# Kernel optimization log

Hardware: AMD Instinct MI355X
Metric: run time of the kernel (lower is better)

The kernel has to match this reference:

```python
import jax, jax.numpy as jnp
import numpy as np

B, L, D_IN = 2, 4096, 512
H, D_K, D_V, D_OUT = 8, 64, 64, 512


def setup_inputs() -> dict:
    key = jax.random.key(0)
    k0, k1, k2, k3, k4 = jax.random.split(key, 5)
    x = jax.random.normal(k0, (B, L, D_IN), dtype=jnp.float32)
    W_q = jax.random.uniform(k1, (H, D_IN, D_K), dtype=jnp.float32)
    W_k = jax.random.uniform(k2, (H, D_IN, D_K), dtype=jnp.float32)
    W_v = jax.random.uniform(k3, (H, D_IN, D_V), dtype=jnp.float32)
    W_o = jax.random.uniform(k4, (H, D_V, D_OUT), dtype=jnp.float32)
    return {"x": x, "W_q": W_q, "W_k": W_k, "W_v": W_v, "W_o": W_o}


def reference(x, W_q, W_k, W_v, W_o):
    # x: (b, l, d_in); projections per head -> (b, h, l, d)
    Q = jnp.einsum('hjk,blj->bhlk', W_q, x)
    K = jnp.einsum('hjk,blj->bhlk', W_k, x)
    V = jnp.einsum('hjv,blj->bhlv', W_v, x)
    # no softmax: pure bilinear attention (Q K^T) V
    scores = jnp.einsum('bhik,bhjk->bhij', Q, K)          # (b, h, l, l)
    values = jnp.einsum('bhqk,bhkv->bhqv', scores, V)     # (b, h, l, d_v)
    return jnp.einsum('hvo,bhlv->blo', W_o, values)       # (b, l, d_out)
```

## Files before the change

### kernel.cpp

```cpp
#include <hip/hip_runtime.h>
#include <cstdint>


#define BDIM 2
#define LDIM 4096
#define DIN 512
#define HDIM 8
#define DK 64
#define DV 64
#define DOUT 512

using bf16_t = __bf16;
typedef __bf16 bf16x8 __attribute__((ext_vector_type(8)));
typedef float floatx4 __attribute__((ext_vector_type(4)));

__device__ __forceinline__ unsigned short f2bf(float f) {
    unsigned int u = __builtin_bit_cast(unsigned int, f);
    u += 0x7FFFu + ((u >> 16) & 1u);
    return (unsigned short)(u >> 16);
}

__device__ __forceinline__ void gld_lds16(const void* g, void* l) {
    __builtin_amdgcn_global_load_lds(
        (const __attribute__((address_space(1))) void*)g,
        (__attribute__((address_space(3))) void*)l, 16, 0, 0);
}

template <int BM, int BN, int BK, bool TRANS_OUT, int OUT_MODE>
__device__ __forceinline__ void gemm_core(const bf16_t* A, const bf16_t* B,
                                          void* Cp, int K, int lda, int ldb,
                                          int ldc, int tm, int tn) {
    constexpr int WM = BM / 2, WN = BN / 2;
    constexpr int FM = WM / 16, FN = WN / 16;
    constexpr int CPR = BK / 8;
    __shared__ bf16_t As[BM * BK];
    __shared__ bf16_t Bs[BN * BK];
    const int tid = threadIdx.x;
    const int lane = tid & 63;
    const int wr = (tid >> 7) & 1;
    const int wc = (tid >> 6) & 1;

    A += (size_t)tm * lda;
    B += (size_t)tn * ldb;

    floatx4 acc[FM][FN] = {};

    for (int k0 = 0; k0 < K; k0 += BK) {
#pragma unroll
        for (int i = 0; i < (BM * CPR) / 256; ++i) {
            int c = i * 256 + tid;
            int m = c / CPR, kc = c % CPR;
            gld_lds16(A + (size_t)m * lda + k0 + kc * 8, As + c * 8);
        }
#pragma unroll
        for (int i = 0; i < (BN * CPR) / 256; ++i) {
            int c = i * 256 + tid;
            int m = c / CPR, kc = c % CPR;
            gld_lds16(B + (size_t)m * ldb + k0 + kc * 8, Bs + c * 8);
        }
        __syncthreads();

#pragma unroll
        for (int kk = 0; kk < BK; kk += 32) {
            bf16x8 aF[FM], bF[FN];
#pragma unroll
            for (int fm = 0; fm < FM; ++fm)
                aF[fm] = *(const bf16x8*)(As + (wr * WM + fm * 16 + (lane & 15)) * BK +
                                          kk + (lane >> 4) * 8);
#pragma unroll
            for (int fn = 0; fn < FN; ++fn)
                bF[fn] = *(const bf16x8*)(Bs + (wc * WN + fn * 16 + (lane & 15)) * BK +
                                          kk + (lane >> 4) * 8);
#pragma unroll
            for (int fm = 0; fm < FM; ++fm)
#pragma unroll
                for (int fn = 0; fn < FN; ++fn)
                    acc[fm][fn] = __builtin_amdgcn_mfma_f32_16x16x32_bf16(
                        aF[fm], bF[fn], acc[fm][fn], 0, 0, 0);
        }
        __syncthreads();
    }

    const int cr4 = (lane >> 4) * 4;
    const int cn = lane & 15;
#pragma unroll
    for (int fm = 0; fm < FM; ++fm)
#pragma unroll
        for (int fn = 0; fn < FN; ++fn)
#pragma unroll
            for (int r = 0; r < 4; ++r) {
                int m = tm + wr * WM + fm * 16 + cr4 + r;
                int n = tn + wc * WN + fn * 16 + cn;
                size_t idx = TRANS_OUT ? ((size_t)n * ldc + m)
                                       : ((size_t)m * ldc + n);
                if (OUT_MODE == 0)
                    ((float*)Cp)[idx] = acc[fm][fn][r];
                else
                    ((unsigned short*)Cp)[idx] = f2bf(acc[fm][fn][r]);
            }
}

__global__ __launch_bounds__(256) void k_kvm(const bf16_t* xb16,
                                             const bf16_t* WkvT, float* M32) {
    constexpr int EP = 136;
    __shared__ bf16_t smem[128 * EP];
    bf16_t* As = smem;
    bf16_t* Bs = smem + 128 * 64;
    const int lt = blockIdx.x, h = blockIdx.y, b = blockIdx.z;
    const int tid = threadIdx.x;
    const int lane = tid & 63;
    const int wr = (tid >> 7) & 1, wc = (tid >> 6) & 1;
    const int cr4 = (lane >> 4) * 4, cn = lane & 15;

    const bf16_t* A = xb16 + (size_t)b * LDIM * DIN + (size_t)lt * 128 * DIN;
    const bf16_t* B = WkvT + (size_t)h * 128 * DIN;

    floatx4 acc[4][4] = {};
    for (int k0 = 0; k0 < DIN; k0 += 64) {
#pragma unroll
        for (int i = 0; i < 4; ++i) {
            int c = i * 256 + tid, m = c >> 3, kc = c & 7;
            gld_lds16(A + (size_t)m * DIN + k0 + kc * 8, As + c * 8);
        }
#pragma unroll
        for (int i = 0; i < 4; ++i) {
            int c = i * 256 + tid, m = c >> 3, kc = c & 7;
            gld_lds16(B + (size_t)m * DIN + k0 + kc * 8, Bs + c * 8);
        }
        __syncthreads();
#pragma unroll
        for (int kk = 0; kk < 64; kk += 32) {
            bf16x8 aF[4], bF[4];
#pragma unroll
            for (int fm = 0; fm < 4; ++fm)
                aF[fm] = *(const bf16x8*)(As + (wr * 64 + fm * 16 + cn) * 64 +
                                          kk + (lane >> 4) * 8);
#pragma unroll
            for (int fn = 0; fn < 4; ++fn)
                bF[fn] = *(const bf16x8*)(Bs + (wc * 64 + fn * 16 + cn) * 64 +
                                          kk + (lane >> 4) * 8);
#pragma unroll
            for (int fm = 0; fm < 4; ++fm)
#pragma unroll
                for (int fn = 0; fn < 4; ++fn)
                    acc[fm][fn] = __builtin_amdgcn_mfma_f32_16x16x32_bf16(
                        aF[fm], bF[fn], acc[fm][fn], 0, 0, 0);
        }
        __syncthreads();
    }

#pragma unroll
    for (int fm = 0; fm < 4; ++fm)
#pragma unroll
        for (int fn = 0; fn < 4; ++fn)
#pragma unroll
            for (int r = 0; r < 4; ++r) {
                int m = wr * 64 + fm * 16 + cr4 + r;
                int n = wc * 64 + fn * 16 + cn;
                ((unsigned short*)smem)[n * EP + m] = f2bf(acc[fm][fn][r]);
            }
    __syncthreads();

    floatx4 mm[2][2] = {};
#pragma unroll
    for (int kk = 0; kk < 128; kk += 32) {
        bf16x8 aF[2], bF[2];
#pragma unroll
        for (int f = 0; f < 2; ++f) {
            aF[f] = *(const bf16x8*)(smem + (wr * 32 + f * 16 + cn) * EP + kk +
                                     (lane >> 4) * 8);
            bF[f] = *(const bf16x8*)(smem + (64 + wc * 32 + f * 16 + cn) * EP +
                                     kk + (lane >> 4) * 8);
        }
#pragma unroll
        for (int fm = 0; fm < 2; ++fm)
#pragma unroll
            for (int fn = 0; fn < 2; ++fn)
                mm[fm][fn] = __builtin_amdgcn_mfma_f32_16x16x32_bf16(
                    aF[fm], bF[fn], mm[fm][fn], 0, 0, 0);
    }
    float* Mh = M32 + ((size_t)(b * HDIM + h)) * (DK * DV);
#pragma unroll
    for (int fm = 0; fm < 2; ++fm)
#pragma unroll
        for (int fn = 0; fn < 2; ++fn)
#pragma unroll
            for (int r = 0; r < 4; ++r) {
                int dk = wr * 32 + fm * 16 + cr4 + r;
                int v = wc * 32 + fn * 16 + cn;
                atomicAdd(&Mh[dk * 64 + v], mm[fm][fn][r]);
            }
}

__global__ __launch_bounds__(256) void k_tail(const bf16_t* WqC, const bf16_t* WoT,
                                              const float* M32, unsigned short* CT) {
    int i0 = blockIdx.x * 64, o0 = blockIdx.y * 64, b = blockIdx.z;
    __shared__ bf16_t Aq[64 * 64];
    __shared__ bf16_t Ws[64 * 64];
    __shared__ bf16_t Msh[64 * 64];
    __shared__ bf16_t PTs[64 * 64];
    const int tid = threadIdx.x;
    const int lane = tid & 63;
    const int wr = (tid >> 7) & 1, wc = (tid >> 6) & 1;
    const int cr4 = (lane >> 4) * 4, cn = lane & 15;

    floatx4 acc[2][2] = {};

    for (int h = 0; h < HDIM; ++h) {
#pragma unroll
        for (int i = 0; i < 2; ++i) {
            int c = i * 256 + tid, m = c >> 3, kc = c & 7;
            gld_lds16(WqC + (size_t)(i0 + m) * DIN + h * 64 + kc * 8, Aq + c * 8);
            gld_lds16(WoT + ((size_t)h * DOUT + o0 + m) * DV + kc * 8, Ws + c * 8);
        }
        const float* Mh = M32 + ((size_t)(b * HDIM + h)) * (DK * DV);
#pragma unroll
        for (int i = 0; i < 4; ++i) {
            int idx = (i * 256 + tid) * 4;
            float4 v = *(const float4*)(Mh + idx);
            *(ushort4*)((unsigned short*)Msh + idx) =
                make_ushort4(f2bf(v.x), f2bf(v.y), f2bf(v.z), f2bf(v.w));
        }
        __syncthreads();

        floatx4 pt[2][2] = {};
#pragma unroll
        for (int kk = 0; kk < 64; kk += 32) {
            bf16x8 aF[2], bF[2];
#pragma unroll
            for (int f = 0; f < 2; ++f) {
                aF[f] = *(const bf16x8*)(Ws + (wr * 32 + f * 16 + cn) * 64 + kk +
                                         (lane >> 4) * 8);
                bF[f] = *(const bf16x8*)(Msh + (wc * 32 + f * 16 + cn) * 64 + kk +
                                         (lane >> 4) * 8);
            }
#pragma unroll
            for (int fm = 0; fm < 2; ++fm)
#pragma unroll
                for (int fn = 0; fn < 2; ++fn)
                    pt[fm][fn] = __builtin_amdgcn_mfma_f32_16x16x32_bf16(
                        aF[fm], bF[fn], pt[fm][fn], 0, 0, 0);
        }
#pragma unroll
        for (int fm = 0; fm < 2; ++fm)
#pragma unroll
            for (int fn = 0; fn < 2; ++fn)
#pragma unroll
                for (int r = 0; r < 4; ++r) {
                    int m = wr * 32 + fm * 16 + cr4 + r;
                    int n = wc * 32 + fn * 16 + cn;
                    ((unsigned short*)PTs)[m * 64 + n] = f2bf(pt[fm][fn][r]);
                }
        __syncthreads();

#pragma unroll
        for (int kk = 0; kk < 64; kk += 32) {
            bf16x8 aF[2], bF[2];
#pragma unroll
            for (int f = 0; f < 2; ++f) {
                aF[f] = *(const bf16x8*)(PTs + (wr * 32 + f * 16 + cn) * 64 + kk +
                                         (lane >> 4) * 8);
                bF[f] = *(const bf16x8*)(Aq + (wc * 32 + f * 16 + cn) * 64 + kk +
                                         (lane >> 4) * 8);
            }
#pragma unroll
            for (int fm = 0; fm < 2; ++fm)
#pragma unroll
                for (int fn = 0; fn < 2; ++fn)
                    acc[fm][fn] = __builtin_amdgcn_mfma_f32_16x16x32_bf16(
                        aF[fm], bF[fn], acc[fm][fn], 0, 0, 0);
        }
        __syncthreads();
    }

    unsigned short* CTb = CT + (size_t)b * DIN * DOUT;
#pragma unroll
    for (int fm = 0; fm < 2; ++fm)
#pragma unroll
        for (int fn = 0; fn < 2; ++fn)
#pragma unroll
            for (int r = 0; r < 4; ++r) {
                int m = wr * 32 + fm * 16 + cr4 + r;
                int n = wc * 32 + fn * 16 + cn;
                CTb[(size_t)(o0 + m) * DIN + i0 + n] = f2bf(acc[fm][fn][r]);
            }
}

__global__ __launch_bounds__(256) void k_out(const bf16_t* x16, const bf16_t* CT,
                                             float* out) {
    int b = blockIdx.z;
    gemm_core<64, 128, 64, false, 0>(x16 + (size_t)b * LDIM * DIN,
                                     CT + (size_t)b * DIN * DOUT,
                                     out + (size_t)b * LDIM * DOUT, DIN, DIN,
                                     DIN, DOUT, blockIdx.x * 64,
                                     blockIdx.y * 128);
}

__global__ __launch_bounds__(256) void k_prep2(
    const float* x, const float* Wq, const float* Wk, const float* Wv,
    const float* Wo, unsigned short* xb, unsigned short* WqC,
    unsigned short* WkvT, unsigned short* WoT, float* M32) {
    __shared__ unsigned short T[64][65];
    int tr = threadIdx.x >> 4, tc4 = (threadIdx.x & 15) * 4;
    int bid = blockIdx.x;
    if (bid < 2048) {
        size_t base = ((size_t)bid * 256 + threadIdx.x) * 8;
        float4 v0 = *(const float4*)(x + base);
        float4 v1 = *(const float4*)(x + base + 4);
        unsigned short o[8] = {f2bf(v0.x), f2bf(v0.y), f2bf(v0.z), f2bf(v0.w),
                               f2bf(v1.x), f2bf(v1.y), f2bf(v1.z), f2bf(v1.w)};
        *(uint4*)(xb + base) = *(const uint4*)o;
        return;
    }
    if (bid >= 2304) {
        size_t g = ((size_t)(bid - 2304) * 256 + threadIdx.x) * 32;
        float4 z4 = make_float4(0.f, 0.f, 0.f, 0.f);
#pragma unroll
        for (int q = 0; q < 8; ++q) *(float4*)(M32 + g + q * 4) = z4;
        return;
    }
    int p_ = bid - 2048;
    int t = p_ & 7, job = (p_ >> 3) & 3, h = p_ >> 5;
    if (job == 0) {
        const float* src = Wq + (size_t)h * DIN * DK;
#pragma unroll
        for (int p = 0; p < 4; ++p) {
            int i = t * 64 + p * 16 + tr;
            float4 v = *(const float4*)(src + (size_t)i * DK + tc4);
            *(ushort4*)(WqC + (size_t)i * (HDIM * DK) + h * DK + tc4) =
                make_ushort4(f2bf(v.x), f2bf(v.y), f2bf(v.z), f2bf(v.w));
        }
        return;
    }
    const float* src;
    unsigned short* dst;
    int rows, cols, r0, c0;
    if (job == 1) {
        src = Wk + (size_t)h * DIN * DK;
        dst = WkvT + ((size_t)h * 128) * DIN;
        rows = DIN; cols = DK; r0 = t * 64; c0 = 0;
    } else if (job == 2) {
        src = Wv + (size_t)h * DIN * DV;
        dst = WkvT + ((size_t)h * 128 + 64) * DIN;
        rows = DIN; cols = DV; r0 = t * 64; c0 = 0;
    } else {
        src = Wo + (size_t)h * DV * DOUT;
        dst = WoT + (size_t)h * DOUT * DV;
        rows = DV; cols = DOUT; r0 = 0; c0 = t * 64;
    }
#pragma unroll
    for (int p = 0; p < 4; ++p) {
        int r = p * 16 + tr;
        float4 v = *(const float4*)(src + (size_t)(r0 + r) * cols + c0 + tc4);
        T[r][tc4 + 0] = f2bf(v.x); T[r][tc4 + 1] = f2bf(v.y);
        T[r][tc4 + 2] = f2bf(v.z); T[r][tc4 + 3] = f2bf(v.w);
    }
    __syncthreads();
#pragma unroll
    for (int p = 0; p < 4; ++p) {
        int c = p * 16 + tr;
        ushort4 u = make_ushort4(T[tc4 + 0][c], T[tc4 + 1][c], T[tc4 + 2][c],
                                 T[tc4 + 3][c]);
        *(ushort4*)(dst + (size_t)(c0 + c) * rows + r0 + tc4) = u;
    }
}

extern "C" void kernel_launch(void* const* d_in, const int* in_sizes, int n_in,
                              void* d_out, int out_size, void* d_ws, size_t ws_size,
                              hipStream_t stream) {
    const float* x  = (const float*)d_in[0];
    const float* Wq = (const float*)d_in[1];
    const float* Wk = (const float*)d_in[2];
    const float* Wv = (const float*)d_in[3];
    const float* Wo = (const float*)d_in[4];
    float* out = (float*)d_out;

    unsigned short* w = (unsigned short*)d_ws;
    unsigned short* xb16  = w; w += (size_t)BDIM * LDIM * DIN;
    unsigned short* WqC   = w; w += (size_t)DIN * HDIM * DK;
    unsigned short* WkvT  = w; w += (size_t)1024 * DIN;
    unsigned short* WoT   = w; w += (size_t)HDIM * DOUT * DV;
    unsigned short* CT    = w; w += (size_t)BDIM * DIN * DOUT;
    float* M32 = (float*)(((uintptr_t)w + 255) & ~(uintptr_t)255);

    k_prep2<<<dim3(2312), 256, 0, stream>>>(x, Wq, Wk, Wv, Wo, xb16, WqC,
                                            WkvT, WoT, M32);
    k_kvm<<<dim3(LDIM / 128, HDIM, BDIM), 256, 0, stream>>>(
        (const bf16_t*)xb16, (const bf16_t*)WkvT, M32);
    k_tail<<<dim3(8, 8, BDIM), 256, 0, stream>>>((const bf16_t*)WqC,
                                                 (const bf16_t*)WoT, M32, CT);
    k_out<<<dim3(LDIM / 64, DOUT / 128, BDIM), 256, 0, stream>>>(
        (const bf16_t*)xb16, (const bf16_t*)CT, out);
}
```

Before: 124.6 us.

## Restructure pipeline around Gram matrix X^T X and fused Q projection

Swaps the per-head K^T V accumulation for a per-batch Gram matrix G = X^T X, computed with atomics over L chunks. The last blocks to finish then wait on a global counter and compute M = Wk^T G Wv per head inside the same kernel, while other blocks of that kernel compute the Q projection. The output kernel now applies M and Wo per head to the stored Q rather than going through a precomputed combined weight. The change adds a transposed copy of x, an inter-block spin-wait that assumes all blocks are co-resident, and a new order of bf16 rounding.

```diff
diff --git a/kernel.cpp b/kernel.cpp
--- a/kernel.cpp
+++ b/kernel.cpp
@@ -9,10 +9,23 @@
 #define DK 64
 #define DV 64
 #define DOUT 512
+#define NXTX 512
+#define NMID 32
+#define SMEM_MAIN 34816
 
 using bf16_t = __bf16;
 typedef __bf16 bf16x8 __attribute__((ext_vector_type(8)));
 typedef float floatx4 __attribute__((ext_vector_type(4)));
+
+constexpr size_t OFF_XB  = 4096;
+constexpr size_t OFF_XT  = OFF_XB  + (size_t)BDIM * LDIM * DIN * 2;
+constexpr size_t OFF_WQT = OFF_XT  + (size_t)BDIM * LDIM * DIN * 2;
+constexpr size_t OFF_WKT = OFF_WQT + (size_t)HDIM * DK * DIN * 2;
+constexpr size_t OFF_WVT = OFF_WKT + (size_t)HDIM * DK * DIN * 2;
+constexpr size_t OFF_WOT = OFF_WVT + (size_t)HDIM * DV * DIN * 2;
+constexpr size_t OFF_QP  = OFF_WOT + (size_t)HDIM * DOUT * DV * 2;
+constexpr size_t OFF_G32 = OFF_QP  + (size_t)BDIM * LDIM * DIN * 2;
+constexpr size_t OFF_M32 = OFF_G32 + (size_t)BDIM * DIN * DIN * 4;
 
 __device__ __forceinline__ unsigned short f2bf(float f) {
     unsigned int u = __builtin_bit_cast(unsigned int, f);
@@ -26,15 +39,16 @@
         (__attribute__((address_space(3))) void*)l, 16, 0, 0);
 }
 
-template <int BM, int BN, int BK, bool TRANS_OUT, int OUT_MODE>
-__device__ __forceinline__ void gemm_core(const bf16_t* A, const bf16_t* B,
-                                          void* Cp, int K, int lda, int ldb,
-                                          int ldc, int tm, int tn) {
+template <int BM, int BN, int BK, int OUT_MODE>
+__device__ __forceinline__ void gemm_tn(char* smem, const bf16_t* A,
+                                        const bf16_t* B, void* Cp, int K,
+                                        int lda, int ldb, int ldc, int tm,
+                                        int tn) {
     constexpr int WM = BM / 2, WN = BN / 2;
     constexpr int FM = WM / 16, FN = WN / 16;
     constexpr int CPR = BK / 8;
-    __shared__ bf16_t As[BM * BK];
-    __shared__ bf16_t Bs[BN * BK];
+    bf16_t* As = (bf16_t*)smem;
+    bf16_t* Bs = As + BM * BK;
     const int tid = threadIdx.x;
     const int lane = tid & 63;
     const int wr = (tid >> 7) & 1;
@@ -91,54 +105,343 @@
             for (int r = 0; r < 4; ++r) {
                 int m = tm + wr * WM + fm * 16 + cr4 + r;
                 int n = tn + wc * WN + fn * 16 + cn;
-                size_t idx = TRANS_OUT ? ((size_t)n * ldc + m)
-                                       : ((size_t)m * ldc + n);
-                if (OUT_MODE == 0)
-                    ((float*)Cp)[idx] = acc[fm][fn][r];
+                size_t idx = (size_t)m * ldc + n;
+                if (OUT_MODE == 1)
+                    ((unsigned short*)Cp)[idx] = f2bf(acc[fm][fn][r]);
                 else
-                    ((unsigned short*)Cp)[idx] = f2bf(acc[fm][fn][r]);
-            }
-}
-
-__global__ __launch_bounds__(256) void k_kvm(const bf16_t* xb16,
-                                             const bf16_t* WkvT, float* M32) {
-    constexpr int EP = 136;
-    __shared__ bf16_t smem[128 * EP];
-    bf16_t* As = smem;
-    bf16_t* Bs = smem + 128 * 64;
-    const int lt = blockIdx.x, h = blockIdx.y, b = blockIdx.z;
+                    atomicAdd((float*)Cp + idx, acc[fm][fn][r]);
+            }
+}
+
+__global__ __launch_bounds__(256) void k_prep(
+    const float* __restrict__ x, const float* __restrict__ Wq,
+    const float* __restrict__ Wk, const float* __restrict__ Wv,
+    const float* __restrict__ Wo, char* __restrict__ ws) {
+    __shared__ unsigned short T[64][65];
+    unsigned short* xb  = (unsigned short*)(ws + OFF_XB);
+    unsigned short* xT  = (unsigned short*)(ws + OFF_XT);
+    unsigned short* WqT = (unsigned short*)(ws + OFF_WQT);
+    unsigned short* WkT = (unsigned short*)(ws + OFF_WKT);
+    unsigned short* WvT = (unsigned short*)(ws + OFF_WVT);
+    unsigned short* WoT = (unsigned short*)(ws + OFF_WOT);
+    float* G32 = (float*)(ws + OFF_G32);
+    float* M32 = (float*)(ws + OFF_M32);
+
     const int tid = threadIdx.x;
-    const int lane = tid & 63;
+    const int tr = tid >> 4, tc4 = (tid & 15) * 4;
+    const int j = blockIdx.x;
+
+    if (j < 1024) {
+        const int b = j >> 9, q = j & 511, lt = q >> 3, it = q & 7;
+        const float* src = x + (size_t)b * LDIM * DIN + (size_t)lt * 64 * DIN +
+                           it * 64;
+        unsigned short* d0 = xb + (size_t)b * LDIM * DIN +
+                             (size_t)lt * 64 * DIN + it * 64;
+        unsigned short* d1 = xT + (size_t)b * DIN * LDIM +
+                             (size_t)it * 64 * LDIM + lt * 64;
+#pragma unroll
+        for (int p = 0; p < 4; ++p) {
+            int r = p * 16 + tr;
+            float4 v = *(const float4*)(src + (size_t)r * DIN + tc4);
+            ushort4 u = make_ushort4(f2bf(v.x), f2bf(v.y), f2bf(v.z), f2bf(v.w));
+            *(ushort4*)(d0 + (size_t)r * DIN + tc4) = u;
+            T[r][tc4 + 0] = u.x; T[r][tc4 + 1] = u.y;
+            T[r][tc4 + 2] = u.z; T[r][tc4 + 3] = u.w;
+        }
+        __syncthreads();
+#pragma unroll
+        for (int p = 0; p < 4; ++p) {
+            int c = p * 16 + tr;
+            ushort4 u = make_ushort4(T[tc4 + 0][c], T[tc4 + 1][c], T[tc4 + 2][c],
+                                     T[tc4 + 3][c]);
+            *(ushort4*)(d1 + (size_t)c * LDIM + tc4) = u;
+        }
+        return;
+    }
+    if (j < 1280) {
+        const int q = j - 1024;
+        const int t = q & 7, h = (q >> 3) & 7, typ = q >> 6;
+        const float* src;
+        unsigned short* dst;
+        int rows, cols, r0, c0;
+        if (typ == 0) { src = Wq + (size_t)h * DIN * DK; dst = WqT + (size_t)h * DK * DIN;
+                        rows = DIN; cols = DK; r0 = t * 64; c0 = 0; }
+        else if (typ == 1) { src = Wk + (size_t)h * DIN * DK; dst = WkT + (size_t)h * DK * DIN;
+                        rows = DIN; cols = DK; r0 = t * 64; c0 = 0; }
+        else if (typ == 2) { src = Wv + (size_t)h * DIN * DV; dst = WvT + (size_t)h * DV * DIN;
+                        rows = DIN; cols = DV; r0 = t * 64; c0 = 0; }
+        else { src = Wo + (size_t)h * DV * DOUT; dst = WoT + (size_t)h * DOUT * DV;
+                        rows = DV; cols = DOUT; r0 = 0; c0 = t * 64; }
+#pragma unroll
+        for (int p = 0; p < 4; ++p) {
+            int r = p * 16 + tr;
+            float4 v = *(const float4*)(src + (size_t)(r0 + r) * cols + c0 + tc4);
+            T[r][tc4 + 0] = f2bf(v.x); T[r][tc4 + 1] = f2bf(v.y);
+            T[r][tc4 + 2] = f2bf(v.z); T[r][tc4 + 3] = f2bf(v.w);
+        }
+        __syncthreads();
+#pragma unroll
+        for (int p = 0; p < 4; ++p) {
+            int c = p * 16 + tr;
+            ushort4 u = make_ushort4(T[tc4 + 0][c], T[tc4 + 1][c], T[tc4 + 2][c],
+                                     T[tc4 + 3][c]);
+            *(ushort4*)(dst + (size_t)(c0 + c) * rows + r0 + tc4) = u;
+        }
+        return;
+    }
+    if (j < 1408) {
+        float* g = G32 + (size_t)(j - 1280) * 8192 + tid * 32;
+        float4 z = make_float4(0.f, 0.f, 0.f, 0.f);
+#pragma unroll
+        for (int q = 0; q < 8; ++q) *(float4*)(g + q * 4) = z;
+        return;
+    }
+    {
+        float* m = M32 + (size_t)(j - 1408) * 8192 + tid * 32;
+        float4 z = make_float4(0.f, 0.f, 0.f, 0.f);
+#pragma unroll
+        for (int q = 0; q < 8; ++q) *(float4*)(m + q * 4) = z;
+        if (j == 1408 && tid == 0) *(unsigned*)ws = 0u;
+    }
+}
+
+__device__ void mid_job(int id, char* smem, const bf16_t* WkT,
+                        const bf16_t* WvT, const float* G32, float* M32) {
+    const int tid = threadIdx.x, lane = tid & 63;
     const int wr = (tid >> 7) & 1, wc = (tid >> 6) & 1;
     const int cr4 = (lane >> 4) * 4, cn = lane & 15;
-
-    const bf16_t* A = xb16 + (size_t)b * LDIM * DIN + (size_t)lt * 128 * DIN;
-    const bf16_t* B = WkvT + (size_t)h * 128 * DIN;
+    const int h = id & 7, b = (id >> 3) & 1, jh = (id >> 4) & 1;
+    bf16_t* As  = (bf16_t*)smem;
+    bf16_t* Bs  = (bf16_t*)(smem + 8192);
+    bf16_t* T2s = (bf16_t*)(smem + 16384);
+    bf16_t* Vs  = (bf16_t*)(smem + 25600);
+    const bf16_t* Ah = WkT + (size_t)h * DK * DIN;
+    const bf16_t* Vh = WvT + (size_t)h * DV * DIN;
+    const float* Gb = G32 + (size_t)b * DIN * DIN;
+
+    floatx4 accM[2][2] = {};
+    for (int jt = 0; jt < 4; ++jt) {
+        const int j0 = jh * 256 + jt * 64;
+        floatx4 accT[2][2] = {};
+        for (int k0 = 0; k0 < DIN; k0 += 64) {
+#pragma unroll
+            for (int i = 0; i < 2; ++i) {
+                int c = i * 256 + tid, m = c >> 3, kc = c & 7;
+                gld_lds16(Ah + (size_t)m * DIN + k0 + kc * 8, As + c * 8);
+            }
+#pragma unroll
+            for (int i = 0; i < 2; ++i) {
+                int c = i * 256 + tid, n = c >> 3, kc = c & 7;
+                const float* g = Gb + (size_t)(j0 + n) * DIN + k0 + kc * 8;
+                float4 v0 = *(const float4*)g;
+                float4 v1 = *(const float4*)(g + 4);
+                unsigned short o[8] = {f2bf(v0.x), f2bf(v0.y), f2bf(v0.z),
+                                       f2bf(v0.w), f2bf(v1.x), f2bf(v1.y),
+                                       f2bf(v1.z), f2bf(v1.w)};
+                *(uint4*)((unsigned short*)Bs + (size_t)c * 8) = *(const uint4*)o;
+            }
+            __syncthreads();
+#pragma unroll
+            for (int kk = 0; kk < 64; kk += 32) {
+                bf16x8 aF[2], bF[2];
+#pragma unroll
+                for (int f = 0; f < 2; ++f) {
+                    aF[f] = *(const bf16x8*)(As + (wr * 32 + f * 16 + cn) * 64 +
+                                             kk + (lane >> 4) * 8);
+                    bF[f] = *(const bf16x8*)(Bs + (wc * 32 + f * 16 + cn) * 64 +
+                                             kk + (lane >> 4) * 8);
+                }
+#pragma unroll
+                for (int fm = 0; fm < 2; ++fm)
+#pragma unroll
+                    for (int fn = 0; fn < 2; ++fn)
+                        accT[fm][fn] = __builtin_amdgcn_mfma_f32_16x16x32_bf16(
+                            aF[fm], bF[fn], accT[fm][fn], 0, 0, 0);
+            }
+            __syncthreads();
+        }
+#pragma unroll
+        for (int fm = 0; fm < 2; ++fm)
+#pragma unroll
+            for (int fn = 0; fn < 2; ++fn)
+#pragma unroll
+                for (int r = 0; r < 4; ++r)
+                    ((unsigned short*)T2s)[(wr * 32 + fm * 16 + cr4 + r) * 72 +
+                                           wc * 32 + fn * 16 + cn] =
+                        f2bf(accT[fm][fn][r]);
+#pragma unroll
+        for (int i = 0; i < 2; ++i) {
+            int c = i * 256 + tid, v = c >> 3, kc = c & 7;
+            gld_lds16(Vh + (size_t)v * DIN + j0 + kc * 8, Vs + c * 8);
+        }
+        __syncthreads();
+#pragma unroll
+        for (int kk = 0; kk < 64; kk += 32) {
+            bf16x8 aF[2], bF[2];
+#pragma unroll
+            for (int f = 0; f < 2; ++f) {
+                aF[f] = *(const bf16x8*)(T2s + (wr * 32 + f * 16 + cn) * 72 + kk +
+                                         (lane >> 4) * 8);
+                bF[f] = *(const bf16x8*)(Vs + (wc * 32 + f * 16 + cn) * 64 + kk +
+                                         (lane >> 4) * 8);
+            }
+#pragma unroll
+            for (int fm = 0; fm < 2; ++fm)
+#pragma unroll
+                for (int fn = 0; fn < 2; ++fn)
+                    accM[fm][fn] = __builtin_amdgcn_mfma_f32_16x16x32_bf16(
+                        aF[fm], bF[fn], accM[fm][fn], 0, 0, 0);
+        }
+        __syncthreads();
+    }
+    float* Mh = M32 + (size_t)(b * HDIM + h) * (DK * DV);
+#pragma unroll
+    for (int fm = 0; fm < 2; ++fm)
+#pragma unroll
+        for (int fn = 0; fn < 2; ++fn)
+#pragma unroll
+            for (int r = 0; r < 4; ++r)
+                atomicAdd(&Mh[(wr * 32 + fm * 16 + cr4 + r) * 64 + wc * 32 +
+                              fn * 16 + cn],
+                          accM[fm][fn][r]);
+}
+
+__global__ __launch_bounds__(256) void k_main(char* __restrict__ ws) {
+    __shared__ __align__(16) char smem[SMEM_MAIN];
+    __shared__ int s_old;
+    const bf16_t* xb  = (const bf16_t*)(ws + OFF_XB);
+    const bf16_t* xT  = (const bf16_t*)(ws + OFF_XT);
+    const bf16_t* WqT = (const bf16_t*)(ws + OFF_WQT);
+    const bf16_t* WkT = (const bf16_t*)(ws + OFF_WKT);
+    const bf16_t* WvT = (const bf16_t*)(ws + OFF_WVT);
+    unsigned short* Qp = (unsigned short*)(ws + OFF_QP);
+    float* G32 = (float*)(ws + OFF_G32);
+    float* M32 = (float*)(ws + OFF_M32);
+    unsigned* done = (unsigned*)ws;
+
+    const int bid = blockIdx.x;
+    const int tid = threadIdx.x;
+
+    if (bid < NXTX) {
+        const int b = bid >> 8, r = bid & 255;
+        const int chunk = r >> 6, t = r & 63;
+        const int it = t >> 3, jt = t & 7;
+        const bf16_t* Xb = xT + (size_t)b * DIN * LDIM + chunk * 1024;
+        gemm_tn<64, 64, 64, 2>(smem, Xb, Xb, G32 + (size_t)b * DIN * DIN, 1024,
+                               LDIM, LDIM, DIN, it * 64, jt * 64);
+        __syncthreads();
+        if (tid == 0) {
+            unsigned old = __hip_atomic_fetch_add(done, 1u, __ATOMIC_RELAXED,
+                                                  __HIP_MEMORY_SCOPE_SYSTEM);
+            s_old = (int)old;
+        }
+        __syncthreads();
+        int old = s_old;
+        if (old >= NXTX - NMID) {
+            if (tid == 0) {
+                while (__hip_atomic_load(done, __ATOMIC_RELAXED,
+                                         __HIP_MEMORY_SCOPE_SYSTEM) <
+                       (unsigned)NXTX)
+                    __builtin_amdgcn_s_sleep(8);
+            }
+            __syncthreads();
+            mid_job(old - (NXTX - NMID), smem, WkT, WvT, G32, M32);
+        }
+    } else {
+        const int q = bid - NXTX;
+        const int b = q >> 7, t = q & 127;
+        const int lt = t >> 2, nt = t & 3;
+        gemm_tn<128, 128, 64, 1>(smem, xb + (size_t)b * LDIM * DIN, WqT,
+                                 Qp + (size_t)b * LDIM * (HDIM * DK), DIN, DIN,
+                                 DIN, HDIM * DK, lt * 128, nt * 128);
+    }
+}
+
+__global__ __launch_bounds__(256) void k_out(const char* __restrict__ ws,
+                                             float* __restrict__ out) {
+    __shared__ __align__(16) bf16_t Qs[128 * 64];
+    __shared__ __align__(16) bf16_t Ws[128 * 64];
+    __shared__ __align__(16) bf16_t Ms[64 * 72];
+    __shared__ __align__(16) bf16_t PTs[128 * 72];
+    const bf16_t* WoT = (const bf16_t*)(ws + OFF_WOT);
+    const bf16_t* Qp  = (const bf16_t*)(ws + OFF_QP);
+    const float* M32  = (const float*)(ws + OFF_M32);
+
+    const int lt = blockIdx.x, nt = blockIdx.y, b = blockIdx.z;
+    const int l0 = lt * 128, o0 = nt * 128;
+    const int tid = threadIdx.x, lane = tid & 63;
+    const int wr = (tid >> 7) & 1, wc = (tid >> 6) & 1;
+    const int cr4 = (lane >> 4) * 4, cn = lane & 15;
 
     floatx4 acc[4][4] = {};
-    for (int k0 = 0; k0 < DIN; k0 += 64) {
+
+    for (int h = 0; h < HDIM; ++h) {
+        {
+            const float* Mh = M32 + (size_t)(b * HDIM + h) * (DK * DV);
+            int dk = tid >> 2, v0 = (tid & 3) * 16;
+            const float* s = Mh + dk * 64 + v0;
+            unsigned short o[16];
+#pragma unroll
+            for (int q = 0; q < 4; ++q) {
+                float4 v = *(const float4*)(s + q * 4);
+                o[q * 4 + 0] = f2bf(v.x); o[q * 4 + 1] = f2bf(v.y);
+                o[q * 4 + 2] = f2bf(v.z); o[q * 4 + 3] = f2bf(v.w);
+            }
+            unsigned short* d = (unsigned short*)Ms + dk * 72 + v0;
+            *(uint4*)d = *(const uint4*)o;
+            *(uint4*)(d + 8) = *(const uint4*)(o + 8);
+        }
 #pragma unroll
         for (int i = 0; i < 4; ++i) {
             int c = i * 256 + tid, m = c >> 3, kc = c & 7;
-            gld_lds16(A + (size_t)m * DIN + k0 + kc * 8, As + c * 8);
-        }
-#pragma unroll
-        for (int i = 0; i < 4; ++i) {
-            int c = i * 256 + tid, m = c >> 3, kc = c & 7;
-            gld_lds16(B + (size_t)m * DIN + k0 + kc * 8, Bs + c * 8);
-        }
-        __syncthreads();
+            gld_lds16(WoT + ((size_t)h * DOUT + o0 + m) * DV + kc * 8,
+                      Ws + c * 8);
+            gld_lds16(Qp + (size_t)b * LDIM * 512 + (size_t)(l0 + m) * 512 +
+                          h * 64 + kc * 8,
+                      Qs + c * 8);
+        }
+        __syncthreads();
+
+        floatx4 accP[2][4] = {};
+#pragma unroll
+        for (int kk = 0; kk < 64; kk += 32) {
+            bf16x8 aF[2], bF[4];
+#pragma unroll
+            for (int f = 0; f < 2; ++f)
+                aF[f] = *(const bf16x8*)(Ms + (wr * 32 + f * 16 + cn) * 72 + kk +
+                                         (lane >> 4) * 8);
+#pragma unroll
+            for (int f = 0; f < 4; ++f)
+                bF[f] = *(const bf16x8*)(Ws + (wc * 64 + f * 16 + cn) * 64 + kk +
+                                         (lane >> 4) * 8);
+#pragma unroll
+            for (int fm = 0; fm < 2; ++fm)
+#pragma unroll
+                for (int fn = 0; fn < 4; ++fn)
+                    accP[fm][fn] = __builtin_amdgcn_mfma_f32_16x16x32_bf16(
+                        aF[fm], bF[fn], accP[fm][fn], 0, 0, 0);
+        }
+#pragma unroll
+        for (int fm = 0; fm < 2; ++fm)
+#pragma unroll
+            for (int fn = 0; fn < 4; ++fn)
+#pragma unroll
+                for (int r = 0; r < 4; ++r)
+                    ((unsigned short*)PTs)[(wc * 64 + fn * 16 + cn) * 72 +
+                                           wr * 32 + fm * 16 + cr4 + r] =
+                        f2bf(accP[fm][fn][r]);
+        __syncthreads();
+
 #pragma unroll
         for (int kk = 0; kk < 64; kk += 32) {
             bf16x8 aF[4], bF[4];
 #pragma unroll
-            for (int fm = 0; fm < 4; ++fm)
-                aF[fm] = *(const bf16x8*)(As + (wr * 64 + fm * 16 + cn) * 64 +
-                                          kk + (lane >> 4) * 8);
-#pragma unroll
-            for (int fn = 0; fn < 4; ++fn)
-                bF[fn] = *(const bf16x8*)(Bs + (wc * 64 + fn * 16 + cn) * 64 +
-                                          kk + (lane >> 4) * 8);
+            for (int f = 0; f < 4; ++f) {
+                aF[f] = *(const bf16x8*)(Qs + (wr * 64 + f * 16 + cn) * 64 + kk +
+                                         (lane >> 4) * 8);
+                bF[f] = *(const bf16x8*)(PTs + (wc * 64 + f * 16 + cn) * 72 + kk +
+                                         (lane >> 4) * 8);
+            }
 #pragma unroll
             for (int fm = 0; fm < 4; ++fm)
 #pragma unroll
@@ -149,220 +452,17 @@
         __syncthreads();
     }
 
+    float* ob = out + (size_t)b * LDIM * DOUT;
 #pragma unroll
     for (int fm = 0; fm < 4; ++fm)
 #pragma unroll
         for (int fn = 0; fn < 4; ++fn)
 #pragma unroll
             for (int r = 0; r < 4; ++r) {
-                int m = wr * 64 + fm * 16 + cr4 + r;
-                int n = wc * 64 + fn * 16 + cn;
-                ((unsigned short*)smem)[n * EP + m] = f2bf(acc[fm][fn][r]);
-            }
-    __syncthreads();
-
-    floatx4 mm[2][2] = {};
-#pragma unroll
-    for (int kk = 0; kk < 128; kk += 32) {
-        bf16x8 aF[2], bF[2];
-#pragma unroll
-        for (int f = 0; f < 2; ++f) {
-            aF[f] = *(const bf16x8*)(smem + (wr * 32 + f * 16 + cn) * EP + kk +
-                                     (lane >> 4) * 8);
-            bF[f] = *(const bf16x8*)(smem + (64 + wc * 32 + f * 16 + cn) * EP +
-                                     kk + (lane >> 4) * 8);
-        }
-#pragma unroll
-        for (int fm = 0; fm < 2; ++fm)
-#pragma unroll
-            for (int fn = 0; fn < 2; ++fn)
-                mm[fm][fn] = __builtin_amdgcn_mfma_f32_16x16x32_bf16(
-                    aF[fm], bF[fn], mm[fm][fn], 0, 0, 0);
-    }
-    float* Mh = M32 + ((size_t)(b * HDIM + h)) * (DK * DV);
-#pragma unroll
-    for (int fm = 0; fm < 2; ++fm)
-#pragma unroll
-        for (int fn = 0; fn < 2; ++fn)
-#pragma unroll
-            for (int r = 0; r < 4; ++r) {
-                int dk = wr * 32 + fm * 16 + cr4 + r;
-                int v = wc * 32 + fn * 16 + cn;
-                atomicAdd(&Mh[dk * 64 + v], mm[fm][fn][r]);
-            }
-}
-
-__global__ __launch_bounds__(256) void k_tail(const bf16_t* WqC, const bf16_t* WoT,
-                                              const float* M32, unsigned short* CT) {
-    int i0 = blockIdx.x * 64, o0 = blockIdx.y * 64, b = blockIdx.z;
-    __shared__ bf16_t Aq[64 * 64];
-    __shared__ bf16_t Ws[64 * 64];
-    __shared__ bf16_t Msh[64 * 64];
-    __shared__ bf16_t PTs[64 * 64];
-    const int tid = threadIdx.x;
-    const int lane = tid & 63;
-    const int wr = (tid >> 7) & 1, wc = (tid >> 6) & 1;
-    const int cr4 = (lane >> 4) * 4, cn = lane & 15;
-
-    floatx4 acc[2][2] = {};
-
-    for (int h = 0; h < HDIM; ++h) {
-#pragma unroll
-        for (int i = 0; i < 2; ++i) {
-            int c = i * 256 + tid, m = c >> 3, kc = c & 7;
-            gld_lds16(WqC + (size_t)(i0 + m) * DIN + h * 64 + kc * 8, Aq + c * 8);
-            gld_lds16(WoT + ((size_t)h * DOUT + o0 + m) * DV + kc * 8, Ws + c * 8);
-        }
-        const float* Mh = M32 + ((size_t)(b * HDIM + h)) * (DK * DV);
-#pragma unroll
-        for (int i = 0; i < 4; ++i) {
-            int idx = (i * 256 + tid) * 4;
-            float4 v = *(const float4*)(Mh + idx);
-            *(ushort4*)((unsigned short*)Msh + idx) =
-                make_ushort4(f2bf(v.x), f2bf(v.y), f2bf(v.z), f2bf(v.w));
-        }
-        __syncthreads();
-
-        floatx4 pt[2][2] = {};
-#pragma unroll
-        for (int kk = 0; kk < 64; kk += 32) {
-            bf16x8 aF[2], bF[2];
-#pragma unroll
-            for (int f = 0; f < 2; ++f) {
-                aF[f] = *(const bf16x8*)(Ws + (wr * 32 + f * 16 + cn) * 64 + kk +
-                                         (lane >> 4) * 8);
-                bF[f] = *(const bf16x8*)(Msh + (wc * 32 + f * 16 + cn) * 64 + kk +
-                                         (lane >> 4) * 8);
-            }
-#pragma unroll
-            for (int fm = 0; fm < 2; ++fm)
-#pragma unroll
-                for (int fn = 0; fn < 2; ++fn)
-                    pt[fm][fn] = __builtin_amdgcn_mfma_f32_16x16x32_bf16(
-                        aF[fm], bF[fn], pt[fm][fn], 0, 0, 0);
-        }
-#pragma unroll
-        for (int fm = 0; fm < 2; ++fm)
-#pragma unroll
-            for (int fn = 0; fn < 2; ++fn)
-#pragma unroll
-                for (int r = 0; r < 4; ++r) {
-                    int m = wr * 32 + fm * 16 + cr4 + r;
-                    int n = wc * 32 + fn * 16 + cn;
-                    ((unsigned short*)PTs)[m * 64 + n] = f2bf(pt[fm][fn][r]);
-                }
-        __syncthreads();
-
-#pragma unroll
-        for (int kk = 0; kk < 64; kk += 32) {
-            bf16x8 aF[2], bF[2];
-#pragma unroll
-            for (int f = 0; f < 2; ++f) {
-                aF[f] = *(const bf16x8*)(PTs + (wr * 32 + f * 16 + cn) * 64 + kk +
-                                         (lane >> 4) * 8);
-                bF[f] = *(const bf16x8*)(Aq + (wc * 32 + f * 16 + cn) * 64 + kk +
-                                         (lane >> 4) * 8);
-            }
-#pragma unroll
-            for (int fm = 0; fm < 2; ++fm)
-#pragma unroll
-                for (int fn = 0; fn < 2; ++fn)
-                    acc[fm][fn] = __builtin_amdgcn_mfma_f32_16x16x32_bf16(
-                        aF[fm], bF[fn], acc[fm][fn], 0, 0, 0);
-        }
-        __syncthreads();
-    }
-
-    unsigned short* CTb = CT + (size_t)b * DIN * DOUT;
-#pragma unroll
-    for (int fm = 0; fm < 2; ++fm)
-#pragma unroll
-        for (int fn = 0; fn < 2; ++fn)
-#pragma unroll
-            for (int r = 0; r < 4; ++r) {
-                int m = wr * 32 + fm * 16 + cr4 + r;
-                int n = wc * 32 + fn * 16 + cn;
-                CTb[(size_t)(o0 + m) * DIN + i0 + n] = f2bf(acc[fm][fn][r]);
-            }
-}
-
-__global__ __launch_bounds__(256) void k_out(const bf16_t* x16, const bf16_t* CT,
-                                             float* out) {
-    int b = blockIdx.z;
-    gemm_core<64, 128, 64, false, 0>(x16 + (size_t)b * LDIM * DIN,
-                                     CT + (size_t)b * DIN * DOUT,
-                                     out + (size_t)b * LDIM * DOUT, DIN, DIN,
-                                     DIN, DOUT, blockIdx.x * 64,
-                                     blockIdx.y * 128);
-}
-
-__global__ __launch_bounds__(256) void k_prep2(
-    const float* x, const float* Wq, const float* Wk, const float* Wv,
-    const float* Wo, unsigned short* xb, unsigned short* WqC,
-    unsigned short* WkvT, unsigned short* WoT, float* M32) {
-    __shared__ unsigned short T[64][65];
-    int tr = threadIdx.x >> 4, tc4 = (threadIdx.x & 15) * 4;
-    int bid = blockIdx.x;
-    if (bid < 2048) {
-        size_t base = ((size_t)bid * 256 + threadIdx.x) * 8;
-        float4 v0 = *(const float4*)(x + base);
-        float4 v1 = *(const float4*)(x + base + 4);
-        unsigned short o[8] = {f2bf(v0.x), f2bf(v0.y), f2bf(v0.z), f2bf(v0.w),
-                               f2bf(v1.x), f2bf(v1.y), f2bf(v1.z), f2bf(v1.w)};
-        *(uint4*)(xb + base) = *(const uint4*)o;
-        return;
-    }
-    if (bid >= 2304) {
-        size_t g = ((size_t)(bid - 2304) * 256 + threadIdx.x) * 32;
-        float4 z4 = make_float4(0.f, 0.f, 0.f, 0.f);
-#pragma unroll
-        for (int q = 0; q < 8; ++q) *(float4*)(M32 + g + q * 4) = z4;
-        return;
-    }
-    int p_ = bid - 2048;
-    int t = p_ & 7, job = (p_ >> 3) & 3, h = p_ >> 5;
-    if (job == 0) {
-        const float* src = Wq + (size_t)h * DIN * DK;
-#pragma unroll
-        for (int p = 0; p < 4; ++p) {
-            int i = t * 64 + p * 16 + tr;
-            float4 v = *(const float4*)(src + (size_t)i * DK + tc4);
-            *(ushort4*)(WqC + (size_t)i * (HDIM * DK) + h * DK + tc4) =
-                make_ushort4(f2bf(v.x), f2bf(v.y), f2bf(v.z), f2bf(v.w));
-        }
-        return;
-    }
-    const float* src;
-    unsigned short* dst;
-    int rows, cols, r0, c0;
-    if (job == 1) {
-        src = Wk + (size_t)h * DIN * DK;
-        dst = WkvT + ((size_t)h * 128) * DIN;
-        rows = DIN; cols = DK; r0 = t * 64; c0 = 0;
-    } else if (job == 2) {
-        src = Wv + (size_t)h * DIN * DV;
-        dst = WkvT + ((size_t)h * 128 + 64) * DIN;
-        rows = DIN; cols = DV; r0 = t * 64; c0 = 0;
-    } else {
-        src = Wo + (size_t)h * DV * DOUT;
-        dst = WoT + (size_t)h * DOUT * DV;
-        rows = DV; cols = DOUT; r0 = 0; c0 = t * 64;
-    }
-#pragma unroll
-    for (int p = 0; p < 4; ++p) {
-        int r = p * 16 + tr;
-        float4 v = *(const float4*)(src + (size_t)(r0 + r) * cols + c0 + tc4);
-        T[r][tc4 + 0] = f2bf(v.x); T[r][tc4 + 1] = f2bf(v.y);
-        T[r][tc4 + 2] = f2bf(v.z); T[r][tc4 + 3] = f2bf(v.w);
-    }
-    __syncthreads();
-#pragma unroll
-    for (int p = 0; p < 4; ++p) {
-        int c = p * 16 + tr;
-        ushort4 u = make_ushort4(T[tc4 + 0][c], T[tc4 + 1][c], T[tc4 + 2][c],
-                                 T[tc4 + 3][c]);
-        *(ushort4*)(dst + (size_t)(c0 + c) * rows + r0 + tc4) = u;
-    }
+                int m = l0 + wr * 64 + fm * 16 + cr4 + r;
+                int n = o0 + wc * 64 + fn * 16 + cn;
+                ob[(size_t)m * DOUT + n] = acc[fm][fn][r];
+            }
 }
 
 extern "C" void kernel_launch(void* const* d_in, const int* in_sizes, int n_in,
@@ -373,22 +473,9 @@
     const float* Wk = (const float*)d_in[2];
     const float* Wv = (const float*)d_in[3];
     const float* Wo = (const float*)d_in[4];
-    float* out = (float*)d_out;
-
-    unsigned short* w = (unsigned short*)d_ws;
-    unsigned short* xb16  = w; w += (size_t)BDIM * LDIM * DIN;
-    unsigned short* WqC   = w; w += (size_t)DIN * HDIM * DK;
-    unsigned short* WkvT  = w; w += (size_t)1024 * DIN;
-    unsigned short* WoT   = w; w += (size_t)HDIM * DOUT * DV;
-    unsigned short* CT    = w; w += (size_t)BDIM * DIN * DOUT;
-    float* M32 = (float*)(((uintptr_t)w + 255) & ~(uintptr_t)255);
-
-    k_prep2<<<dim3(2312), 256, 0, stream>>>(x, Wq, Wk, Wv, Wo, xb16, WqC,
-                                            WkvT, WoT, M32);
-    k_kvm<<<dim3(LDIM / 128, HDIM, BDIM), 256, 0, stream>>>(
-        (const bf16_t*)xb16, (const bf16_t*)WkvT, M32);
-    k_tail<<<dim3(8, 8, BDIM), 256, 0, stream>>>((const bf16_t*)WqC,
-                                                 (const bf16_t*)WoT, M32, CT);
-    k_out<<<dim3(LDIM / 64, DOUT / 128, BDIM), 256, 0, stream>>>(
-        (const bf16_t*)xb16, (const bf16_t*)CT, out);
-}
+
+    k_prep<<<dim3(1416), 256, 0, stream>>>(x, Wq, Wk, Wv, Wo, (char*)d_ws);
+    k_main<<<dim3(768), 256, 0, stream>>>((char*)d_ws);
+    k_out<<<dim3(32, 4, BDIM), 256, 0, stream>>>((const char*)d_ws,
+                                                 (float*)d_out);
+}
```

Result: slower. 163.6 us (+31.3%).
